# Kernel tuning notes

Measured on AMD Instinct MI355X. Metric: run time of the kernel, lower is better.

The kernel has to match this reference:

```python
import jax, jax.numpy as jnp
import numpy as np

N, D, C = 4096, 1024, 1000
EPS = 1e-8


def _remove_diag(M):
    # faithful to torch M[off_diag_mask].view(h, h-1) via strided-reshape trick
    h = M.shape[0]
    return M.reshape(-1)[1:].reshape(h - 1, h + 1)[:, :-1].reshape(h, h - 1)


def _cosine_sim_matrix(x, y):
    # torch CosineSimilarity: x.y / max(||x||*||y||, eps)
    xn = jnp.linalg.norm(x, axis=-1, keepdims=True)
    yn = jnp.linalg.norm(y, axis=-1, keepdims=True)
    num = jnp.einsum('id,jd->ij', x, y)
    den = jnp.maximum(xn * yn.T, EPS)
    return num / den


def setup_inputs() -> dict:
    key = jax.random.key(0)
    k1, k2, k3, k4 = jax.random.split(key, 4)
    return {
        'inst_embed': jax.random.normal(k1, (N, D), dtype=jnp.float32),
        'anchor': jax.random.normal(k2, (N, D), dtype=jnp.float32),
        'cls_mask': jax.random.randint(k3, (C, N), 0, 2, dtype=jnp.int32),
        'labels': jax.random.randint(k4, (N,), 0, C, dtype=jnp.int64),
        'temperature': jnp.float32(1.0),
    }


def reference(inst_embed, anchor, cls_mask, labels, temperature):
    # augmentation=None branch of Conditional_Embedding_Contrastive_loss.forward
    sim = _cosine_sim_matrix(inst_embed, inst_embed)          # [N,N]
    instance_zone = jnp.exp(_remove_diag(sim) / temperature)  # [N,N-1]
    mask_neg = _remove_diag(cls_mask[labels].astype(instance_zone.dtype))  # [N,N-1]
    inst2inst_pos = instance_zone * mask_neg
    # elementwise cosine sim between inst_embed and anchor rows
    dot = jnp.sum(inst_embed * anchor, axis=-1)
    nrm = jnp.maximum(jnp.linalg.norm(inst_embed, axis=-1) * jnp.linalg.norm(anchor, axis=-1), EPS)
    inst2embed_pos = jnp.exp((dot / nrm) / temperature)       # [N]
    numerator = inst2inst_pos.sum(axis=1) + inst2embed_pos
    denominator = inst2embed_pos + instance_zone.sum(axis=1)
    return -jnp.mean(jnp.log(numerator / denominator))
```

## Files before the change

### kernel.cpp

```cpp
#include <hip/hip_runtime.h>
#include <hip/hip_bf16.h>
#include <math.h>


#define NN   4096
#define DD   1024
#define NCLS 1000
#define EPSF 1e-8f
#define MW   (NN / 32)
#define NTILE 528
#define SLOTS 32

typedef short bf16x8 __attribute__((ext_vector_type(8)));
typedef float f32x4  __attribute__((ext_vector_type(4)));

__global__ __launch_bounds__(256) void k_pack(const int* __restrict__ cmask,
                                              const int* __restrict__ lraw,
                                              unsigned int* __restrict__ mbits,
                                              int* __restrict__ lab) {
  const int b = blockIdx.x;
  if (b < NCLS * MW / 256) {
    const int wword = b * 256 + threadIdx.x;
    const int* src = cmask + (size_t)wword * 32;
    unsigned int v = 0;
    #pragma unroll
    for (int q = 0; q < 8; ++q) {
      const int4 c = *(const int4*)(src + q * 4);
      v |= (c.x != 0 ? 1u : 0u) << (q * 4 + 0);
      v |= (c.y != 0 ? 1u : 0u) << (q * 4 + 1);
      v |= (c.z != 0 ? 1u : 0u) << (q * 4 + 2);
      v |= (c.w != 0 ? 1u : 0u) << (q * 4 + 3);
    }
    mbits[wword] = v;
  } else {
    __shared__ int stride_s;
    if (threadIdx.x == 0) {
      int stride = 2;
      #pragma unroll
      for (int t = 0; t < 8; ++t) {
        int lo = lraw[2 * t], hi = lraw[2 * t + 1];
        if (hi != 0 || (unsigned)lo >= (unsigned)NCLS) { stride = 1; break; }
      }
      stride_s = stride;
    }
    __syncthreads();
    const int i = (b - NCLS * MW / 256) * 256 + threadIdx.x;
    lab[i] = lraw[i * stride_s];
  }
}

__global__ __launch_bounds__(256) void k_rowstats(
    const float* __restrict__ X, const float* __restrict__ A,
    const float* __restrict__ Tp, ushort* __restrict__ Xb,
    float* __restrict__ rnx, float* __restrict__ rnT,
    float* __restrict__ epos, float* __restrict__ out) {
  const int i = blockIdx.x;
  const int t = threadIdx.x;
  const size_t base = (size_t)i * DD + t * 4;
  const float4 xv = *(const float4*)(X + base);
  const float4 av = *(const float4*)(A + base);
  float sxx = xv.x * xv.x + xv.y * xv.y + xv.z * xv.z + xv.w * xv.w;
  float saa = av.x * av.x + av.y * av.y + av.z * av.z + av.w * av.w;
  float sxa = xv.x * av.x + xv.y * av.y + xv.z * av.z + xv.w * av.w;

  ushort4 pk;
  { __hip_bfloat16 b;
    b = __float2bfloat16(xv.x); pk.x = *(const ushort*)&b;
    b = __float2bfloat16(xv.y); pk.y = *(const ushort*)&b;
    b = __float2bfloat16(xv.z); pk.z = *(const ushort*)&b;
    b = __float2bfloat16(xv.w); pk.w = *(const ushort*)&b; }
  *(ushort4*)(Xb + base) = pk;

  #pragma unroll
  for (int off = 32; off > 0; off >>= 1) {
    sxx += __shfl_down(sxx, off);
    saa += __shfl_down(saa, off);
    sxa += __shfl_down(sxa, off);
  }
  __shared__ float red[3][4];
  const int w = t >> 6;
  if ((t & 63) == 0) { red[0][w] = sxx; red[1][w] = saa; red[2][w] = sxa; }
  __syncthreads();
  if (t == 0) {
    const float a  = red[0][0] + red[0][1] + red[0][2] + red[0][3];
    const float bb = red[1][0] + red[1][1] + red[1][2] + red[1][3];
    const float c  = red[2][0] + red[2][1] + red[2][2] + red[2][3];
    const float nxi = sqrtf(a), nai = sqrtf(bb);
    const float rT  = 1.0f / Tp[0];
    const float r   = 1.0f / fmaxf(nxi, 1e-20f);
    rnx[i] = r;
    rnT[i] = r * rT;
    epos[i] = expf((c / fmaxf(nxi * nai, EPSF)) * rT);
    if (i == 0) out[0] = 0.f;
  }
}

#define BM 128
#define BK 64

__global__ __launch_bounds__(256) void k_gram(
    const ushort* __restrict__ Xb, const float* __restrict__ rnx,
    const float* __restrict__ rnT,
    const int* __restrict__ lab, const unsigned int* __restrict__ mbits,
    float* __restrict__ scrF, float* __restrict__ scrM) {
  __shared__ __align__(16) char As[BM * BK * 2];
  __shared__ __align__(16) char Bs[BM * BK * 2];
  const int tid  = threadIdx.x;
  const int lane = tid & 63;
  const int w    = tid >> 6;
  const int wr   = w >> 1, wc = w & 1;

  const int xcd = blockIdx.x & 7;
  const int l   = blockIdx.x >> 3;
  const int p   = (xcd << 1) + (l >= 33);
  const int q   = (l >= 33) ? (l - 33) : l;
  int by, bx;
  if (q < 32 - p) { by = p;      bx = p + q; }
  else            { by = 31 - p; bx = 31 - p + (q - (32 - p)); }
  const bool offdiag = (bx != by);
  const int i0 = by * BM;
  const int j0 = bx * BM;

  const int sslot = (lane & 7) ^ (lane >> 3);

  f32x4 acc[4][4];
  #pragma unroll
  for (int m = 0; m < 4; ++m)
    #pragma unroll
    for (int n = 0; n < 4; ++n)
      acc[m][n] = (f32x4){0.f, 0.f, 0.f, 0.f};

  const ushort* pA[4];
  const ushort* pB[4];
  #pragma unroll
  for (int q2 = 0; q2 < 4; ++q2) {
    const int row = q2 * 32 + w * 8 + (lane >> 3);
    pA[q2] = Xb + (size_t)(i0 + row) * DD + sslot * 8;
    pB[q2] = Xb + (size_t)(j0 + row) * DD + sslot * 8;
  }

  for (int k0 = 0; k0 < DD; k0 += BK) {
    #pragma unroll
    for (int q2 = 0; q2 < 4; ++q2) {
      __builtin_amdgcn_global_load_lds(
          (const __attribute__((address_space(1))) void*)(pA[q2] + k0),
          (__attribute__((address_space(3))) void*)(As + (q2 * 4 + w) * 1024), 16, 0, 0);
      __builtin_amdgcn_global_load_lds(
          (const __attribute__((address_space(1))) void*)(pB[q2] + k0),
          (__attribute__((address_space(3))) void*)(Bs + (q2 * 4 + w) * 1024), 16, 0, 0);
    }
    __syncthreads();

    #pragma unroll
    for (int ks = 0; ks < 2; ++ks) {
      const int slot = ((ks << 2) + (lane >> 4)) ^ (lane & 7);
      bf16x8 af[4], bfr[4];
      #pragma unroll
      for (int m = 0; m < 4; ++m) {
        const int r = (wr << 6) + (m << 4) + (lane & 15);
        af[m] = *(const bf16x8*)(As + r * 128 + (slot << 4));
      }
      #pragma unroll
      for (int n = 0; n < 4; ++n) {
        const int r = (wc << 6) + (n << 4) + (lane & 15);
        bfr[n] = *(const bf16x8*)(Bs + r * 128 + (slot << 4));
      }
      #pragma unroll
      for (int m = 0; m < 4; ++m)
        #pragma unroll
        for (int n = 0; n < 4; ++n)
          acc[m][n] = __builtin_amdgcn_mfma_f32_16x16x32_bf16(af[m], bfr[n], acc[m][n], 0, 0, 0);
    }
    __syncthreads();
  }

  float* LF = (float*)As;
  float* LM = LF + 256;
  float* GF = LM + 256;
  float* GM = GF + 256;

  float rnT_j[4];
  unsigned long long wj[4];
  #pragma unroll
  for (int n = 0; n < 4; ++n) {
    const int j = j0 + (wc << 6) + (n << 4) + (lane & 15);
    rnT_j[n] = rnT[j];
    wj[n] = *(const unsigned long long*)(mbits + (size_t)lab[j] * MW + (i0 >> 5) + (wr << 1));
  }
  float pse[4] = {0.f, 0.f, 0.f, 0.f}, psm[4] = {0.f, 0.f, 0.f, 0.f};

  #pragma unroll
  for (int m = 0; m < 4; ++m) {
    #pragma unroll
    for (int r = 0; r < 4; ++r) {
      const int irow = (m << 4) + ((lane >> 4) << 2) + r;
      const int i = i0 + (wr << 6) + irow;
      const float rni = rnx[i];
      const unsigned long long wi =
          *(const unsigned long long*)(mbits + (size_t)lab[i] * MW + (j0 >> 5) + (wc << 1));
      float se = 0.f, sm = 0.f;
      #pragma unroll
      for (int n = 0; n < 4; ++n) {
        const int j = j0 + (wc << 6) + (n << 4) + (lane & 15);
        float e = __expf(acc[m][n][r] * rni * rnT_j[n]);
        if (i == j) e = 0.f;
        se += e;
        const int bposj = (n << 4) + (lane & 15);
        sm += ((wi >> bposj) & 1ull) ? e : 0.f;
        pse[n] += e;
        psm[n] += ((wj[n] >> irow) & 1ull) ? e : 0.f;
      }
      #pragma unroll
      for (int off = 1; off < 16; off <<= 1) {
        se += __shfl_xor(se, off);
        sm += __shfl_xor(sm, off);
      }
      if ((lane & 15) == 0) {
        LF[(wc << 7) + (wr << 6) + irow] = se;
        LM[(wc << 7) + (wr << 6) + irow] = sm;
      }
    }
  }
  if (offdiag) {
    #pragma unroll
    for (int n = 0; n < 4; ++n) {
      float se = pse[n], sm = psm[n];
      se += __shfl_xor(se, 16); se += __shfl_xor(se, 32);
      sm += __shfl_xor(sm, 16); sm += __shfl_xor(sm, 32);
      if (lane < 16) {
        GF[(wr << 7) + (wc << 6) + (n << 4) + lane] = se;
        GM[(wr << 7) + (wc << 6) + (n << 4) + lane] = sm;
      }
    }
  }
  __syncthreads();

  if (tid < 128) {
    scrF[(size_t)bx * NN + i0 + tid] = LF[tid] + LF[128 + tid];
    if (offdiag) scrF[(size_t)by * NN + j0 + tid] = GF[tid] + GF[128 + tid];
  } else {
    const int u = tid - 128;
    scrM[(size_t)bx * NN + i0 + u] = LM[u] + LM[128 + u];
    if (offdiag) scrM[(size_t)by * NN + j0 + u] = GM[u] + GM[128 + u];
  }
}

__global__ __launch_bounds__(256) void k_final(
    const float* __restrict__ scrF, const float* __restrict__ scrM,
    const float* __restrict__ epos, float* __restrict__ out) {
  const int idx = blockIdx.x * 256 + threadIdx.x;
  float sf = 0.f, sm = 0.f;
  #pragma unroll
  for (int s = 0; s < SLOTS; ++s) {
    sf += scrF[(size_t)s * NN + idx];
    sm += scrM[(size_t)s * NN + idx];
  }
  const float ep  = epos[idx];
  const float num = sm + ep;
  const float den = ep + sf;
  float v = (logf(den) - logf(num)) * (1.0f / (float)NN);
  #pragma unroll
  for (int off = 32; off > 0; off >>= 1) v += __shfl_down(v, off);
  __shared__ float red[4];
  if ((threadIdx.x & 63) == 0) red[threadIdx.x >> 6] = v;
  __syncthreads();
  if (threadIdx.x == 0) atomicAdd(out, red[0] + red[1] + red[2] + red[3]);
}

extern "C" void kernel_launch(void* const* d_in, const int* in_sizes, int n_in,
                              void* d_out, int out_size, void* d_ws, size_t ws_size,
                              hipStream_t stream) {
  const float* X     = (const float*)d_in[0];
  const float* A     = (const float*)d_in[1];
  const int*   cmask = (const int*)d_in[2];
  const int*   lraw  = (const int*)d_in[3];
  const float* Tp    = (const float*)d_in[4];
  float* out = (float*)d_out;

  char* ws = (char*)d_ws;
  ushort* Xb   = (ushort*)ws;
  float* rnx   = (float*)(ws + (size_t)NN * DD * 2);
  float* rnT   = rnx + NN;
  float* epos  = rnT + NN;
  int*   lab   = (int*)(epos + NN);
  unsigned int* mbits = (unsigned int*)(lab + NN);
  float* scrF  = (float*)(mbits + (size_t)NCLS * MW);
  float* scrM  = scrF + (size_t)SLOTS * NN;

  hipLaunchKernelGGL(k_pack,     dim3(NCLS * MW / 256 + NN / 256), dim3(256), 0, stream, cmask, lraw, mbits, lab);
  hipLaunchKernelGGL(k_rowstats, dim3(NN),    dim3(256), 0, stream, X, A, Tp, Xb, rnx, rnT, epos, out);
  hipLaunchKernelGGL(k_gram,     dim3(NTILE), dim3(256), 0, stream, Xb, rnx, rnT, lab, mbits, scrF, scrM);
  hipLaunchKernelGGL(k_final,    dim3(NN/256), dim3(256), 0, stream, scrF, scrM, epos, out);
}
```

Baseline: 83.51 us.

## Replace symmetric 128-tile Gram with full 256-tile, 4-stage pipelined MFMA kernel

After: 82.47 us. Within noise of the previous version (-1.3%).

```diff
diff --git a/kernel.cpp b/kernel.cpp
--- a/kernel.cpp
+++ b/kernel.cpp
@@ -8,19 +8,62 @@
 #define NCLS 1000
 #define EPSF 1e-8f
 #define MW   (NN / 32)
-#define NTILE 528
-#define SLOTS 32
+#define SLOTS 16
+#define NT   32
 
 typedef short bf16x8 __attribute__((ext_vector_type(8)));
 typedef float f32x4  __attribute__((ext_vector_type(4)));
 
-__global__ __launch_bounds__(256) void k_pack(const int* __restrict__ cmask,
-                                              const int* __restrict__ lraw,
-                                              unsigned int* __restrict__ mbits,
-                                              int* __restrict__ lab) {
+__global__ __launch_bounds__(256) void k_prep(
+    const float* __restrict__ X, const float* __restrict__ A,
+    const float* __restrict__ Tp, const int* __restrict__ cmask,
+    const int* __restrict__ lraw,
+    ushort* __restrict__ Xb, float* __restrict__ rnx, float* __restrict__ rnT,
+    float* __restrict__ epos, unsigned int* __restrict__ mbits,
+    int* __restrict__ lab, float* __restrict__ out) {
   const int b = blockIdx.x;
-  if (b < NCLS * MW / 256) {
-    const int wword = b * 256 + threadIdx.x;
+  if (b < NN) {
+    const int i = b;
+    const int t = threadIdx.x;
+    const size_t base = (size_t)i * DD + t * 4;
+    const float4 xv = *(const float4*)(X + base);
+    const float4 av = *(const float4*)(A + base);
+    float sxx = xv.x * xv.x + xv.y * xv.y + xv.z * xv.z + xv.w * xv.w;
+    float saa = av.x * av.x + av.y * av.y + av.z * av.z + av.w * av.w;
+    float sxa = xv.x * av.x + xv.y * av.y + xv.z * av.z + xv.w * av.w;
+
+    ushort4 pk;
+    { __hip_bfloat16 bb;
+      bb = __float2bfloat16(xv.x); pk.x = *(const ushort*)&bb;
+      bb = __float2bfloat16(xv.y); pk.y = *(const ushort*)&bb;
+      bb = __float2bfloat16(xv.z); pk.z = *(const ushort*)&bb;
+      bb = __float2bfloat16(xv.w); pk.w = *(const ushort*)&bb; }
+    *(ushort4*)(Xb + base) = pk;
+
+    #pragma unroll
+    for (int off = 32; off > 0; off >>= 1) {
+      sxx += __shfl_down(sxx, off);
+      saa += __shfl_down(saa, off);
+      sxa += __shfl_down(sxa, off);
+    }
+    __shared__ float red[3][4];
+    const int w = t >> 6;
+    if ((t & 63) == 0) { red[0][w] = sxx; red[1][w] = saa; red[2][w] = sxa; }
+    __syncthreads();
+    if (t == 0) {
+      const float a  = red[0][0] + red[0][1] + red[0][2] + red[0][3];
+      const float b2 = red[1][0] + red[1][1] + red[1][2] + red[1][3];
+      const float c  = red[2][0] + red[2][1] + red[2][2] + red[2][3];
+      const float nxi = sqrtf(a), nai = sqrtf(b2);
+      const float rT  = 1.0f / Tp[0];
+      const float r   = 1.0f / fmaxf(nxi, 1e-20f);
+      rnx[i] = r;
+      rnT[i] = r * rT;
+      epos[i] = expf((c / fmaxf(nxi * nai, EPSF)) * rT);
+      if (i == 0) out[0] = 0.f;
+    }
+  } else if (b < NN + NCLS * MW / 256) {
+    const int wword = (b - NN) * 256 + threadIdx.x;
     const int* src = cmask + (size_t)wword * 32;
     unsigned int v = 0;
     #pragma unroll
@@ -44,157 +87,115 @@
       stride_s = stride;
     }
     __syncthreads();
-    const int i = (b - NCLS * MW / 256) * 256 + threadIdx.x;
+    const int i = (b - NN - NCLS * MW / 256) * 256 + threadIdx.x;
     lab[i] = lraw[i * stride_s];
   }
 }
 
-__global__ __launch_bounds__(256) void k_rowstats(
-    const float* __restrict__ X, const float* __restrict__ A,
-    const float* __restrict__ Tp, ushort* __restrict__ Xb,
-    float* __restrict__ rnx, float* __restrict__ rnT,
-    float* __restrict__ epos, float* __restrict__ out) {
-  const int i = blockIdx.x;
-  const int t = threadIdx.x;
-  const size_t base = (size_t)i * DD + t * 4;
-  const float4 xv = *(const float4*)(X + base);
-  const float4 av = *(const float4*)(A + base);
-  float sxx = xv.x * xv.x + xv.y * xv.y + xv.z * xv.z + xv.w * xv.w;
-  float saa = av.x * av.x + av.y * av.y + av.z * av.z + av.w * av.w;
-  float sxa = xv.x * av.x + xv.y * av.y + xv.z * av.z + xv.w * av.w;
-
-  ushort4 pk;
-  { __hip_bfloat16 b;
-    b = __float2bfloat16(xv.x); pk.x = *(const ushort*)&b;
-    b = __float2bfloat16(xv.y); pk.y = *(const ushort*)&b;
-    b = __float2bfloat16(xv.z); pk.z = *(const ushort*)&b;
-    b = __float2bfloat16(xv.w); pk.w = *(const ushort*)&b; }
-  *(ushort4*)(Xb + base) = pk;
-
-  #pragma unroll
-  for (int off = 32; off > 0; off >>= 1) {
-    sxx += __shfl_down(sxx, off);
-    saa += __shfl_down(saa, off);
-    sxa += __shfl_down(sxa, off);
-  }
-  __shared__ float red[3][4];
-  const int w = t >> 6;
-  if ((t & 63) == 0) { red[0][w] = sxx; red[1][w] = saa; red[2][w] = sxa; }
-  __syncthreads();
-  if (t == 0) {
-    const float a  = red[0][0] + red[0][1] + red[0][2] + red[0][3];
-    const float bb = red[1][0] + red[1][1] + red[1][2] + red[1][3];
-    const float c  = red[2][0] + red[2][1] + red[2][2] + red[2][3];
-    const float nxi = sqrtf(a), nai = sqrtf(bb);
-    const float rT  = 1.0f / Tp[0];
-    const float r   = 1.0f / fmaxf(nxi, 1e-20f);
-    rnx[i] = r;
-    rnT[i] = r * rT;
-    epos[i] = expf((c / fmaxf(nxi * nai, EPSF)) * rT);
-    if (i == 0) out[0] = 0.f;
-  }
-}
-
-#define BM 128
-#define BK 64
-
-__global__ __launch_bounds__(256) void k_gram(
+
+__global__ __launch_bounds__(512, 2) void k_gram(
     const ushort* __restrict__ Xb, const float* __restrict__ rnx,
     const float* __restrict__ rnT,
     const int* __restrict__ lab, const unsigned int* __restrict__ mbits,
     float* __restrict__ scrF, float* __restrict__ scrM) {
-  __shared__ __align__(16) char As[BM * BK * 2];
-  __shared__ __align__(16) char Bs[BM * BK * 2];
+  __shared__ __align__(16) char LDS[4 * 32768];
   const int tid  = threadIdx.x;
   const int lane = tid & 63;
   const int w    = tid >> 6;
-  const int wr   = w >> 1, wc = w & 1;
+  const int wr   = w >> 2;
+  const int wc   = w & 3;
 
   const int xcd = blockIdx.x & 7;
-  const int l   = blockIdx.x >> 3;
-  const int p   = (xcd << 1) + (l >= 33);
-  const int q   = (l >= 33) ? (l - 33) : l;
-  int by, bx;
-  if (q < 32 - p) { by = p;      bx = p + q; }
-  else            { by = 31 - p; bx = 31 - p + (q - (32 - p)); }
-  const bool offdiag = (bx != by);
-  const int i0 = by * BM;
-  const int j0 = bx * BM;
-
-  const int sslot = (lane & 7) ^ (lane >> 3);
-
-  f32x4 acc[4][4];
-  #pragma unroll
-  for (int m = 0; m < 4; ++m)
+  const int idx = blockIdx.x >> 3;
+  const int by  = (xcd << 1) + (idx >> 4);
+  const int bx  = idx & 15;
+  const int i0 = by * 256;
+  const int j0 = bx * 256;
+
+  const int srow = ((w & 3) << 6) + lane;
+  const ushort* gA = Xb + (size_t)(i0 + srow) * DD + (w >> 2) * 8;
+  const ushort* gB = Xb + (size_t)(j0 + srow) * DD + (w >> 2) * 8;
+  const int dOff = ((w >> 2) << 12) + ((w & 3) << 10);
+
+  #define STAGE(T)                                                              \
+    {                                                                           \
+      char* bp = LDS + ((T) & 3) * 32768;                                       \
+      const int k0e = (T) * 32;                                                 \
+      __builtin_amdgcn_global_load_lds(                                         \
+          (const __attribute__((address_space(1))) void*)(gA + k0e),            \
+          (__attribute__((address_space(3))) void*)(bp + dOff), 16, 0, 0);      \
+      __builtin_amdgcn_global_load_lds(                                         \
+          (const __attribute__((address_space(1))) void*)(gA + k0e + 16),       \
+          (__attribute__((address_space(3))) void*)(bp + dOff + 8192), 16, 0, 0); \
+      __builtin_amdgcn_global_load_lds(                                         \
+          (const __attribute__((address_space(1))) void*)(gB + k0e),            \
+          (__attribute__((address_space(3))) void*)(bp + 16384 + dOff), 16, 0, 0); \
+      __builtin_amdgcn_global_load_lds(                                         \
+          (const __attribute__((address_space(1))) void*)(gB + k0e + 16),       \
+          (__attribute__((address_space(3))) void*)(bp + 16384 + dOff + 8192), 16, 0, 0); \
+    }
+
+  int aoff[8], boff[4];
+  #pragma unroll
+  for (int m = 0; m < 8; ++m)
+    aoff[m] = ((lane >> 4) << 12) + (((wr << 7) + (m << 4) + (lane & 15)) << 4);
+  #pragma unroll
+  for (int n = 0; n < 4; ++n)
+    boff[n] = 16384 + ((lane >> 4) << 12) + (((wc << 6) + (n << 4) + (lane & 15)) << 4);
+
+  f32x4 acc[8][4];
+  #pragma unroll
+  for (int m = 0; m < 8; ++m)
     #pragma unroll
     for (int n = 0; n < 4; ++n)
       acc[m][n] = (f32x4){0.f, 0.f, 0.f, 0.f};
 
-  const ushort* pA[4];
-  const ushort* pB[4];
-  #pragma unroll
-  for (int q2 = 0; q2 < 4; ++q2) {
-    const int row = q2 * 32 + w * 8 + (lane >> 3);
-    pA[q2] = Xb + (size_t)(i0 + row) * DD + sslot * 8;
-    pB[q2] = Xb + (size_t)(j0 + row) * DD + sslot * 8;
-  }
-
-  for (int k0 = 0; k0 < DD; k0 += BK) {
-    #pragma unroll
-    for (int q2 = 0; q2 < 4; ++q2) {
-      __builtin_amdgcn_global_load_lds(
-          (const __attribute__((address_space(1))) void*)(pA[q2] + k0),
-          (__attribute__((address_space(3))) void*)(As + (q2 * 4 + w) * 1024), 16, 0, 0);
-      __builtin_amdgcn_global_load_lds(
-          (const __attribute__((address_space(1))) void*)(pB[q2] + k0),
-          (__attribute__((address_space(3))) void*)(Bs + (q2 * 4 + w) * 1024), 16, 0, 0);
-    }
-    __syncthreads();
-
-    #pragma unroll
-    for (int ks = 0; ks < 2; ++ks) {
-      const int slot = ((ks << 2) + (lane >> 4)) ^ (lane & 7);
-      bf16x8 af[4], bfr[4];
-      #pragma unroll
-      for (int m = 0; m < 4; ++m) {
-        const int r = (wr << 6) + (m << 4) + (lane & 15);
-        af[m] = *(const bf16x8*)(As + r * 128 + (slot << 4));
-      }
-      #pragma unroll
-      for (int n = 0; n < 4; ++n) {
-        const int r = (wc << 6) + (n << 4) + (lane & 15);
-        bfr[n] = *(const bf16x8*)(Bs + r * 128 + (slot << 4));
-      }
-      #pragma unroll
-      for (int m = 0; m < 4; ++m)
-        #pragma unroll
-        for (int n = 0; n < 4; ++n)
-          acc[m][n] = __builtin_amdgcn_mfma_f32_16x16x32_bf16(af[m], bfr[n], acc[m][n], 0, 0, 0);
-    }
-    __syncthreads();
-  }
-
-  float* LF = (float*)As;
-  float* LM = LF + 256;
-  float* GF = LM + 256;
-  float* GM = GF + 256;
+  #define COMPUTE(T)                                                            \
+    {                                                                           \
+      const char* bp = LDS + ((T) & 3) * 32768;                                 \
+      bf16x8 af[8], bfr[4];                                                     \
+      _Pragma("unroll")                                                         \
+      for (int n = 0; n < 4; ++n) bfr[n] = *(const bf16x8*)(bp + boff[n]);      \
+      _Pragma("unroll")                                                         \
+      for (int m = 0; m < 8; ++m) af[m] = *(const bf16x8*)(bp + aoff[m]);       \
+      __builtin_amdgcn_s_setprio(1);                                            \
+      _Pragma("unroll")                                                         \
+      for (int m = 0; m < 8; ++m)                                               \
+        _Pragma("unroll")                                                       \
+        for (int n = 0; n < 4; ++n)                                             \
+          acc[m][n] = __builtin_amdgcn_mfma_f32_16x16x32_bf16(af[m], bfr[n], acc[m][n], 0, 0, 0); \
+      __builtin_amdgcn_s_setprio(0);                                            \
+    }
+
+  STAGE(0) STAGE(1) STAGE(2)
+
+  for (int t = 0; t <= NT - 4; ++t) {
+    asm volatile("s_waitcnt vmcnt(8)\n\ts_barrier" ::: "memory");
+    STAGE(t + 3)
+    COMPUTE(t)
+  }
+  asm volatile("s_waitcnt vmcnt(8)\n\ts_barrier" ::: "memory");
+  COMPUTE(29)
+  asm volatile("s_waitcnt vmcnt(4)\n\ts_barrier" ::: "memory");
+  COMPUTE(30)
+  asm volatile("s_waitcnt vmcnt(0)\n\ts_barrier" ::: "memory");
+  COMPUTE(31)
+  __syncthreads();
+
+  float* LF = (float*)LDS;
+  float* LM = LF + 1024;
 
   float rnT_j[4];
-  unsigned long long wj[4];
-  #pragma unroll
-  for (int n = 0; n < 4; ++n) {
-    const int j = j0 + (wc << 6) + (n << 4) + (lane & 15);
-    rnT_j[n] = rnT[j];
-    wj[n] = *(const unsigned long long*)(mbits + (size_t)lab[j] * MW + (i0 >> 5) + (wr << 1));
-  }
-  float pse[4] = {0.f, 0.f, 0.f, 0.f}, psm[4] = {0.f, 0.f, 0.f, 0.f};
-
-  #pragma unroll
-  for (int m = 0; m < 4; ++m) {
+  #pragma unroll
+  for (int n = 0; n < 4; ++n)
+    rnT_j[n] = rnT[j0 + (wc << 6) + (n << 4) + (lane & 15)];
+
+  #pragma unroll
+  for (int m = 0; m < 8; ++m) {
     #pragma unroll
     for (int r = 0; r < 4; ++r) {
       const int irow = (m << 4) + ((lane >> 4) << 2) + r;
-      const int i = i0 + (wr << 6) + irow;
+      const int i = i0 + (wr << 7) + irow;
       const float rni = rnx[i];
       const unsigned long long wi =
           *(const unsigned long long*)(mbits + (size_t)lab[i] * MW + (j0 >> 5) + (wc << 1));
@@ -207,8 +208,6 @@
         se += e;
         const int bposj = (n << 4) + (lane & 15);
         sm += ((wi >> bposj) & 1ull) ? e : 0.f;
-        pse[n] += e;
-        psm[n] += ((wj[n] >> irow) & 1ull) ? e : 0.f;
       }
       #pragma unroll
       for (int off = 1; off < 16; off <<= 1) {
@@ -216,32 +215,18 @@
         sm += __shfl_xor(sm, off);
       }
       if ((lane & 15) == 0) {
-        LF[(wc << 7) + (wr << 6) + irow] = se;
-        LM[(wc << 7) + (wr << 6) + irow] = sm;
-      }
-    }
-  }
-  if (offdiag) {
-    #pragma unroll
-    for (int n = 0; n < 4; ++n) {
-      float se = pse[n], sm = psm[n];
-      se += __shfl_xor(se, 16); se += __shfl_xor(se, 32);
-      sm += __shfl_xor(sm, 16); sm += __shfl_xor(sm, 32);
-      if (lane < 16) {
-        GF[(wr << 7) + (wc << 6) + (n << 4) + lane] = se;
-        GM[(wr << 7) + (wc << 6) + (n << 4) + lane] = sm;
+        LF[(wc << 8) + (wr << 7) + irow] = se;
+        LM[(wc << 8) + (wr << 7) + irow] = sm;
       }
     }
   }
   __syncthreads();
 
-  if (tid < 128) {
-    scrF[(size_t)bx * NN + i0 + tid] = LF[tid] + LF[128 + tid];
-    if (offdiag) scrF[(size_t)by * NN + j0 + tid] = GF[tid] + GF[128 + tid];
+  if (tid < 256) {
+    scrF[(size_t)bx * NN + i0 + tid] = LF[tid] + LF[256 + tid] + LF[512 + tid] + LF[768 + tid];
   } else {
-    const int u = tid - 128;
-    scrM[(size_t)bx * NN + i0 + u] = LM[u] + LM[128 + u];
-    if (offdiag) scrM[(size_t)by * NN + j0 + u] = GM[u] + GM[128 + u];
+    const int u = tid - 256;
+    scrM[(size_t)bx * NN + i0 + u] = LM[u] + LM[256 + u] + LM[512 + u] + LM[768 + u];
   }
 }
 
@@ -287,8 +272,11 @@
   float* scrF  = (float*)(mbits + (size_t)NCLS * MW);
   float* scrM  = scrF + (size_t)SLOTS * NN;
 
-  hipLaunchKernelGGL(k_pack,     dim3(NCLS * MW / 256 + NN / 256), dim3(256), 0, stream, cmask, lraw, mbits, lab);
-  hipLaunchKernelGGL(k_rowstats, dim3(NN),    dim3(256), 0, stream, X, A, Tp, Xb, rnx, rnT, epos, out);
-  hipLaunchKernelGGL(k_gram,     dim3(NTILE), dim3(256), 0, stream, Xb, rnx, rnT, lab, mbits, scrF, scrM);
-  hipLaunchKernelGGL(k_final,    dim3(NN/256), dim3(256), 0, stream, scrF, scrM, epos, out);
-}
+  const int prepg = NN + NCLS * MW / 256 + NN / 256;
+
+  hipLaunchKernelGGL(k_prep,  dim3(prepg),  dim3(256), 0, stream,
+                     X, A, Tp, cmask, lraw, Xb, rnx, rnT, epos, mbits, lab, out);
+  hipLaunchKernelGGL(k_gram,  dim3(256),    dim3(512), 0, stream,
+                     Xb, rnx, rnT, lab, mbits, scrF, scrM);
+  hipLaunchKernelGGL(k_final, dim3(NN/256), dim3(256), 0, stream, scrF, scrM, epos, out);
+}
```
